# Kernel tuning notes

Measured on AMD Instinct MI355X. Metric: run time of the kernel, lower is better.

## Reference

```python
import jax, jax.numpy as jnp
import numpy as np

N, E, D = 50000, 1600000, 128


def _mk_w(key, shape):
    return jax.random.normal(key, shape, dtype=jnp.float32) * 0.05


def setup_inputs() -> dict:
    key = jax.random.key(0)
    ks = jax.random.split(key, 32)
    inp = {
        'x_in': jax.random.normal(ks[0], (N, D), dtype=jnp.float32),
        'rows': jax.random.randint(ks[1], (E,), 0, N, dtype=jnp.int64 if jax.config.jax_enable_x64 else jnp.int32),
        'cols': jax.random.randint(ks[2], (E,), 0, N, dtype=jnp.int64 if jax.config.jax_enable_x64 else jnp.int32),
        'vals': jax.random.uniform(ks[3], (E,), dtype=jnp.float32),
    }
    names = ['m1_W1', 'm1_W2', 'm2_W1', 'm2_W2', 'Wu1', 'Wu2', 'Wr1', 'Wr2', 'Wo1', 'Wo2']
    for i, n in enumerate(names):
        inp[n] = _mk_w(ks[4 + i], (D, D))
        inp[n.replace('W', 'b')] = jnp.zeros((D,), dtype=jnp.float32)
    return inp


def _mlp2(x, W1, b1, W2, b2):
    # 2-layer MLP: Linear -> ReLU -> Linear
    return jax.nn.relu(x @ W1 + b1) @ W2 + b2


def reference(x_in, rows, cols, vals,
              m1_W1, m1_b1, m1_W2, m1_b2,
              m2_W1, m2_b1, m2_W2, m2_b2,
              Wu1, bu1, Wu2, bu2,
              Wr1, br1, Wr2, br2,
              Wo1, bo1, Wo2, bo2):
    x = _mlp2(x_in, m1_W1, m1_b1, m1_W2, m1_b2)            # [N, D]
    # sparse COO spmm: out[i] = sum_e vals[e] * x[cols[e]] for rows[e] == i
    msgs = vals[:, None] * x[cols]                          # [E, D]
    agg = jax.ops.segment_sum(msgs, rows, num_segments=N)   # [N, D]
    out = _mlp2(agg, m2_W1, m2_b1, m2_W2, m2_b2)
    z = jax.nn.sigmoid(out @ Wu1 + bu1 + x @ Wu2 + bu2)
    r = jax.nn.sigmoid(out @ Wr1 + br1 + x @ Wr2 + br2)
    h = jnp.tanh(out @ Wo1 + bo1 + (r * x) @ Wo2 + bo2)
    return (1.0 - z) * x + z * h
```

## Files before the change

kernel.cpp:

```cpp
#include <hip/hip_runtime.h>

#define DD 128
#define BSHIFT 7
#define BROWS 128
#define MS_TILE 4096
#define MS_EPT 8
#define STAGE_CAP 6144

typedef __attribute__((ext_vector_type(8))) short short8;
typedef __attribute__((ext_vector_type(4))) float f32x4;
typedef unsigned short u16;
typedef unsigned int u32;

__device__ __forceinline__ u16 f2bf(float f) {
  u32 u = __builtin_bit_cast(u32, f);
  u += 0x7fffu + ((u >> 16) & 1u);
  return (u16)(u >> 16);
}
__device__ __forceinline__ float bf2f(u16 s) {
  u32 u = ((u32)s) << 16;
  return __builtin_bit_cast(float, u);
}
__device__ __forceinline__ float f16val(u32 cv) {
  return (float)__builtin_bit_cast(_Float16, (u16)(cv & 0xffffu));
}
__device__ __forceinline__ float sigmoidf_(float v) { return 1.f / (1.f + __expf(-v)); }
__device__ __forceinline__ float tanhf_(float v) {
  float e = __expf(-2.f * v);
  return (1.f - e) / (1.f + e);
}

struct WPtrs { const float* w[10]; };

__global__ void pack_weights(WPtrs wp, u16* __restrict__ bp) {
  const float* W = wp.w[blockIdx.x];
  u16* out = bp + (size_t)blockIdx.x * 16384;
  for (int o = threadIdx.x; o < 16384; o += blockDim.x) {
    int e = o & 7, lane = (o >> 3) & 63, nt = (o >> 9) & 7, ks = o >> 12;
    int k = ks * 32 + (lane >> 4) * 8 + e;
    int c = (lane & 15) + nt * 16;
    out[o] = f2bf(W[k * DD + c]);
  }
}

__global__ __launch_bounds__(512) void multisplit(const int* __restrict__ rows,
                                                  const int* __restrict__ cols,
                                                  const float* __restrict__ vals,
                                                  int* __restrict__ cursor,
                                                  uint2* __restrict__ recs,
                                                  int E, int NB, int cap) {
  __shared__ u32 hist[512];
  __shared__ u32 scan_tmp[512];
  __shared__ u32 hbase[512];
  __shared__ int gbase[512];
  __shared__ u32 rankc[512];
  __shared__ uint2 stage[MS_TILE];
  const int t = threadIdx.x;
  const int tile0 = blockIdx.x * MS_TILE;
  hist[t] = 0;
  rankc[t] = 0;
  __syncthreads();
  int myb[MS_EPT];
  u32 mycv[MS_EPT], myrow[MS_EPT];
#pragma unroll
  for (int j = 0; j < MS_EPT; ++j) {
    int e = tile0 + j * 512 + t;
    if (e < E) {
      int r = rows[e];
      int b = r >> BSHIFT;
      myb[j] = b;
      myrow[j] = (u32)r;
      _Float16 hf = (_Float16)vals[e];
      mycv[j] = ((u32)cols[e] << 16) | (u32)__builtin_bit_cast(u16, hf);
      atomicAdd(&hist[b], 1u);
    } else {
      myb[j] = -1;
    }
  }
  __syncthreads();
  u32 v = hist[t];
  scan_tmp[t] = v;
  __syncthreads();
  for (int o = 1; o < 512; o <<= 1) {
    u32 x = (t >= o) ? scan_tmp[t - o] : 0;
    __syncthreads();
    scan_tmp[t] += x;
    __syncthreads();
  }
  hbase[t] = scan_tmp[t] - v;
  if (t < NB && v > 0) gbase[t] = atomicAdd(&cursor[t], (int)v);
  __syncthreads();
#pragma unroll
  for (int j = 0; j < MS_EPT; ++j) {
    if (myb[j] >= 0) {
      u32 rk = atomicAdd(&rankc[myb[j]], 1u);
      stage[hbase[myb[j]] + rk].x = mycv[j];
      stage[hbase[myb[j]] + rk].y = myrow[j];
    }
  }
  __syncthreads();
  int cnt = E - tile0;
  cnt = cnt < MS_TILE ? cnt : MS_TILE;
  for (int k = t; k < cnt; k += 512) {
    uint2 rec = stage[k];
    int b = (int)(rec.y >> BSHIFT);
    int off = gbase[b] + (k - (int)hbase[b]);
    if (off < cap) recs[(size_t)b * cap + off] = rec;
  }
}

__global__ __launch_bounds__(512) void bucket_csr(const uint2* __restrict__ recs,
                                                  const int* __restrict__ cursor,
                                                  u32* __restrict__ recs2,
                                                  int* __restrict__ rowstart,
                                                  int* __restrict__ rowcnt, int n, int cap) {
  __shared__ int hist[BROWS];
  __shared__ int sc[BROWS];
  __shared__ int hbase[BROWS];
  __shared__ u32 rank[BROWS];
  __shared__ u32 stage[STAGE_CAP];
  const int t = threadIdx.x;
  const int b = blockIdx.x;
  int cnt = cursor[b];
  cnt = cnt < cap ? cnt : cap;
  const uint2* rb = recs + (size_t)b * cap;
  if (t < BROWS) { hist[t] = 0; rank[t] = 0; }
  __syncthreads();
  for (int i = t; i < cnt; i += 512) atomicAdd(&hist[rb[i].y & (BROWS - 1)], 1);
  __syncthreads();
  if (t < BROWS) sc[t] = hist[t];
  __syncthreads();
  for (int o = 1; o < BROWS; o <<= 1) {
    int x = (t >= o && t < BROWS) ? sc[t - o] : 0;
    __syncthreads();
    if (t < BROWS) sc[t] += x;
    __syncthreads();
  }
  if (t < BROWS) {
    hbase[t] = sc[t] - hist[t];
    int r = (b << BSHIFT) + t;
    if (r < n) {
      rowstart[r] = b * cap + hbase[t];
      rowcnt[r] = hist[t];
    }
  }
  __syncthreads();
  for (int i = t; i < cnt; i += 512) {
    uint2 rec = rb[i];
    int lr = (int)(rec.y & (BROWS - 1));
    u32 p = atomicAdd(&rank[lr], 1u);
    stage[hbase[lr] + p] = rec.x;
  }
  __syncthreads();
  u32* ob = recs2 + (size_t)b * cap;
  for (int i = t; i < cnt; i += 512) ob[i] = stage[i];
}

__global__ void spmm_agg(const int* __restrict__ rowstart, const int* __restrict__ rowcnt,
                         const u32* __restrict__ recs2, const u16* __restrict__ xb,
                         u16* __restrict__ aggb, int n) {
  int row = blockIdx.x * 4 + (threadIdx.x >> 6);
  int lane = threadIdx.x & 63;
  if (row >= n) return;
  int s = rowstart[row];
  int e2 = s + rowcnt[row];
  float a0 = 0.f, a1 = 0.f;
  int j = s;
  for (; j + 3 < e2; j += 4) {
    u32 pk0 = recs2[j], pk1 = recs2[j + 1], pk2 = recs2[j + 2], pk3 = recs2[j + 3];
    u32 x0 = *reinterpret_cast<const u32*>(xb + (size_t)(pk0 >> 16) * DD + lane * 2);
    u32 x1 = *reinterpret_cast<const u32*>(xb + (size_t)(pk1 >> 16) * DD + lane * 2);
    u32 x2 = *reinterpret_cast<const u32*>(xb + (size_t)(pk2 >> 16) * DD + lane * 2);
    u32 x3 = *reinterpret_cast<const u32*>(xb + (size_t)(pk3 >> 16) * DD + lane * 2);
    float v0 = f16val(pk0), v1 = f16val(pk1), v2 = f16val(pk2), v3 = f16val(pk3);
    a0 += v0 * bf2f((u16)(x0 & 0xffff)) + v1 * bf2f((u16)(x1 & 0xffff)) +
          v2 * bf2f((u16)(x2 & 0xffff)) + v3 * bf2f((u16)(x3 & 0xffff));
    a1 += v0 * bf2f((u16)(x0 >> 16)) + v1 * bf2f((u16)(x1 >> 16)) +
          v2 * bf2f((u16)(x2 >> 16)) + v3 * bf2f((u16)(x3 >> 16));
  }
  for (; j < e2; ++j) {
    u32 pk = recs2[j];
    u32 x0 = *reinterpret_cast<const u32*>(xb + (size_t)(pk >> 16) * DD + lane * 2);
    float v0 = f16val(pk);
    a0 += v0 * bf2f((u16)(x0 & 0xffff));
    a1 += v0 * bf2f((u16)(x0 >> 16));
  }
  u32 o = ((u32)f2bf(a1) << 16) | (u32)f2bf(a0);
  *reinterpret_cast<u32*>(aggb + (size_t)row * DD + lane * 2) = o;
}

template <int ASRC>
__global__ __launch_bounds__(256) void mlp_fused(const void* __restrict__ Ain,
                                                 const u16* __restrict__ W1p,
                                                 const float* __restrict__ b1,
                                                 const u16* __restrict__ W2p,
                                                 const float* __restrict__ b2,
                                                 u16* __restrict__ outB, int n) {
  __shared__ u16 sm[32][136];
  const int lane = threadIdx.x & 63;
  const int wid = threadIdx.x >> 6;
  const int m = wid >> 1, c = wid & 1;
  const int row0 = blockIdx.x * 32 + m * 16;
  const int ar = lane & 15, ak = (lane >> 4) * 8;
  const int crow = 4 * (lane >> 4), ccol = lane & 15;

  f32x4 acc[4];
#pragma unroll
  for (int t = 0; t < 4; ++t) acc[t] = f32x4{0.f, 0.f, 0.f, 0.f};

#pragma unroll
  for (int ks = 0; ks < 4; ++ks) {
    short8 a;
    int r = row0 + ar;
    r = r < n ? r : n - 1;
    if (ASRC == 0) {
      const float* Ap = (const float*)Ain + (size_t)r * DD + ks * 32 + ak;
      float4 f0 = *reinterpret_cast<const float4*>(Ap);
      float4 f1 = *reinterpret_cast<const float4*>(Ap + 4);
      short8 tv;
      tv[0] = (short)f2bf(f0.x); tv[1] = (short)f2bf(f0.y);
      tv[2] = (short)f2bf(f0.z); tv[3] = (short)f2bf(f0.w);
      tv[4] = (short)f2bf(f1.x); tv[5] = (short)f2bf(f1.y);
      tv[6] = (short)f2bf(f1.z); tv[7] = (short)f2bf(f1.w);
      a = tv;
    } else {
      a = *reinterpret_cast<const short8*>((const u16*)Ain + (size_t)r * DD + ks * 32 + ak);
    }
#pragma unroll
    for (int nt4 = 0; nt4 < 4; ++nt4) {
      int nt = c * 4 + nt4;
      short8 bfr = *reinterpret_cast<const short8*>(W1p + (((ks * 8 + nt) * 64 + lane) * 8));
      acc[nt4] = __builtin_amdgcn_mfma_f32_16x16x32_bf16(a, bfr, acc[nt4], 0, 0, 0);
    }
  }
#pragma unroll
  for (int nt4 = 0; nt4 < 4; ++nt4) {
    int col = (c * 4 + nt4) * 16 + ccol;
    float bsv = b1[col];
#pragma unroll
    for (int e = 0; e < 4; ++e) {
      float v = acc[nt4][e] + bsv;
      v = v > 0.f ? v : 0.f;
      sm[m * 16 + crow + e][col] = f2bf(v);
    }
  }
  __syncthreads();

  f32x4 acc2[4];
#pragma unroll
  for (int t = 0; t < 4; ++t) acc2[t] = f32x4{0.f, 0.f, 0.f, 0.f};
#pragma unroll
  for (int ks = 0; ks < 4; ++ks) {
    short8 a2 = *reinterpret_cast<const short8*>(&sm[m * 16 + ar][ks * 32 + ak]);
#pragma unroll
    for (int nt4 = 0; nt4 < 4; ++nt4) {
      int nt = c * 4 + nt4;
      short8 bfr = *reinterpret_cast<const short8*>(W2p + (((ks * 8 + nt) * 64 + lane) * 8));
      acc2[nt4] = __builtin_amdgcn_mfma_f32_16x16x32_bf16(a2, bfr, acc2[nt4], 0, 0, 0);
    }
  }
#pragma unroll
  for (int nt4 = 0; nt4 < 4; ++nt4) {
    int col = (c * 4 + nt4) * 16 + ccol;
    float bsv = b2[col];
#pragma unroll
    for (int e = 0; e < 4; ++e) {
      int r = row0 + crow + e;
      if (r < n) outB[(size_t)r * DD + col] = f2bf(acc2[nt4][e] + bsv);
    }
  }
}

__global__ __launch_bounds__(256) void gates_final(
    const u16* __restrict__ Ao, const u16* __restrict__ Ax, const u16* __restrict__ Wu1p,
    const u16* __restrict__ Wu2p, const u16* __restrict__ Wr1p, const u16* __restrict__ Wr2p,
    const u16* __restrict__ Wo1p, const u16* __restrict__ Wo2p, const float* __restrict__ bu1,
    const float* __restrict__ bu2, const float* __restrict__ br1, const float* __restrict__ br2,
    const float* __restrict__ bo1, const float* __restrict__ bo2, float* __restrict__ out,
    int n) {
  __shared__ u16 sm[32][136];
  const int lane = threadIdx.x & 63;
  const int wid = threadIdx.x >> 6;
  const int m = wid >> 1, c = wid & 1;
  const int row0 = blockIdx.x * 32 + m * 16;
  const int ar = lane & 15, ak = (lane >> 4) * 8;
  const int crow = 4 * (lane >> 4), ccol = lane & 15;

  f32x4 aZ[4], aR[4], aO[4];
#pragma unroll
  for (int t = 0; t < 4; ++t) {
    aZ[t] = f32x4{0.f, 0.f, 0.f, 0.f};
    aR[t] = f32x4{0.f, 0.f, 0.f, 0.f};
    aO[t] = f32x4{0.f, 0.f, 0.f, 0.f};
  }
#pragma unroll
  for (int ks = 0; ks < 4; ++ks) {
    int r = row0 + ar;
    r = r < n ? r : n - 1;
    short8 ao = *reinterpret_cast<const short8*>(Ao + (size_t)r * DD + ks * 32 + ak);
    short8 ax = *reinterpret_cast<const short8*>(Ax + (size_t)r * DD + ks * 32 + ak);
#pragma unroll
    for (int nt4 = 0; nt4 < 4; ++nt4) {
      int nt = c * 4 + nt4;
      size_t bo = (size_t)(((ks * 8 + nt) * 64 + lane) * 8);
      short8 b1 = *reinterpret_cast<const short8*>(Wu1p + bo);
      short8 b2 = *reinterpret_cast<const short8*>(Wu2p + bo);
      short8 b3 = *reinterpret_cast<const short8*>(Wr1p + bo);
      short8 b4 = *reinterpret_cast<const short8*>(Wr2p + bo);
      short8 b5 = *reinterpret_cast<const short8*>(Wo1p + bo);
      aZ[nt4] = __builtin_amdgcn_mfma_f32_16x16x32_bf16(ao, b1, aZ[nt4], 0, 0, 0);
      aZ[nt4] = __builtin_amdgcn_mfma_f32_16x16x32_bf16(ax, b2, aZ[nt4], 0, 0, 0);
      aR[nt4] = __builtin_amdgcn_mfma_f32_16x16x32_bf16(ao, b3, aR[nt4], 0, 0, 0);
      aR[nt4] = __builtin_amdgcn_mfma_f32_16x16x32_bf16(ax, b4, aR[nt4], 0, 0, 0);
      aO[nt4] = __builtin_amdgcn_mfma_f32_16x16x32_bf16(ao, b5, aO[nt4], 0, 0, 0);
    }
  }
#pragma unroll
  for (int nt4 = 0; nt4 < 4; ++nt4) {
    int col = (c * 4 + nt4) * 16 + ccol;
    float bz = bu1[col] + bu2[col];
    float br_ = br1[col] + br2[col];
    float bo_ = bo1[col];
#pragma unroll
    for (int e = 0; e < 4; ++e) {
      int r = row0 + crow + e;
      float z = sigmoidf_(aZ[nt4][e] + bz);
      float rr = sigmoidf_(aR[nt4][e] + br_);
      aZ[nt4][e] = z;
      aO[nt4][e] = aO[nt4][e] + bo_;
      float xv = 0.f;
      if (r < n) xv = bf2f(Ax[(size_t)r * DD + col]);
      sm[m * 16 + crow + e][col] = f2bf(rr * xv);
    }
  }
  __syncthreads();

  f32x4 acc2[4];
#pragma unroll
  for (int t = 0; t < 4; ++t) acc2[t] = f32x4{0.f, 0.f, 0.f, 0.f};
#pragma unroll
  for (int ks = 0; ks < 4; ++ks) {
    short8 a2 = *reinterpret_cast<const short8*>(&sm[m * 16 + ar][ks * 32 + ak]);
#pragma unroll
    for (int nt4 = 0; nt4 < 4; ++nt4) {
      int nt = c * 4 + nt4;
      short8 bfr = *reinterpret_cast<const short8*>(Wo2p + (((ks * 8 + nt) * 64 + lane) * 8));
      acc2[nt4] = __builtin_amdgcn_mfma_f32_16x16x32_bf16(a2, bfr, acc2[nt4], 0, 0, 0);
    }
  }
#pragma unroll
  for (int nt4 = 0; nt4 < 4; ++nt4) {
    int col = (c * 4 + nt4) * 16 + ccol;
    float bo2v = bo2[col];
#pragma unroll
    for (int e = 0; e < 4; ++e) {
      int r = row0 + crow + e;
      if (r < n) {
        size_t idx = (size_t)r * DD + col;
        float oi = acc2[nt4][e] + bo2v + aO[nt4][e];
        float h = tanhf_(oi);
        float z = aZ[nt4][e];
        float xv = bf2f(Ax[idx]);
        out[idx] = (1.f - z) * xv + z * h;
      }
    }
  }
}

extern "C" void kernel_launch(void* const* d_in, const int* in_sizes, int n_in,
                              void* d_out, int out_size, void* d_ws, size_t ws_size,
                              hipStream_t stream) {
  const int n = in_sizes[0] / DD;
  const int E = in_sizes[1];
  const float* x_in = (const float*)d_in[0];
  const int* rows = (const int*)d_in[1];
  const int* cols = (const int*)d_in[2];
  const float* vals = (const float*)d_in[3];
  const float* Wm[10];
  const float* Bm[10];
  for (int i = 0; i < 10; ++i) {
    Wm[i] = (const float*)d_in[4 + 2 * i];
    Bm[i] = (const float*)d_in[5 + 2 * i];
  }

  const int NB = (n + BROWS - 1) >> BSHIFT;
  int cap = (((E / NB) * 5) / 4 + 511) & ~511;
  cap = cap < STAGE_CAP ? cap : STAGE_CAP;

  char* base = (char*)d_ws;
  size_t off = 0;
  auto alloc = [&](size_t bytes) -> char* {
    char* p = base + off;
    off += (bytes + 255) & ~(size_t)255;
    return p;
  };
  u16* wpack = (u16*)alloc((size_t)10 * 16384 * 2);
  u16* x_b = (u16*)alloc((size_t)n * DD * 2);
  u16* agg_b = (u16*)alloc((size_t)n * DD * 2);
  int* cursor = (int*)alloc((size_t)NB * 4);
  int* rowstart = (int*)alloc((size_t)n * 4);
  int* rowcnt = (int*)alloc((size_t)n * 4);
  uint2* recs = (uint2*)alloc((size_t)NB * cap * 8);
  u32* recs2 = (u32*)alloc((size_t)NB * cap * 4);
  (void)ws_size;
  (void)n_in;
  (void)out_size;

  hipMemsetAsync(cursor, 0, (size_t)NB * 4, stream);
  WPtrs wp;
  for (int i = 0; i < 10; ++i) wp.w[i] = Wm[i];
  pack_weights<<<10, 256, 0, stream>>>(wp, wpack);
  multisplit<<<(E + MS_TILE - 1) / MS_TILE, 512, 0, stream>>>(rows, cols, vals, cursor, recs, E,
                                                             NB, cap);
  bucket_csr<<<NB, 512, 0, stream>>>(recs, cursor, recs2, rowstart, rowcnt, n, cap);
  int gblocks = (n + 31) / 32;
  mlp_fused<0><<<gblocks, 256, 0, stream>>>(x_in, wpack + 0 * 16384, Bm[0], wpack + 1 * 16384,
                                            Bm[1], x_b, n);
  spmm_agg<<<(n + 3) / 4, 256, 0, stream>>>(rowstart, rowcnt, recs2, x_b, agg_b, n);
  mlp_fused<1><<<gblocks, 256, 0, stream>>>(agg_b, wpack + 2 * 16384, Bm[2], wpack + 3 * 16384,
                                            Bm[3], agg_b, n);
  gates_final<<<gblocks, 256, 0, stream>>>(
      agg_b, x_b, wpack + 4 * 16384, wpack + 5 * 16384, wpack + 6 * 16384, wpack + 7 * 16384,
      wpack + 8 * 16384, wpack + 9 * 16384, Bm[4], Bm[5], Bm[6], Bm[7], Bm[8], Bm[9],
      (float*)d_out, n);
}
```

Before: 306.1 us.

## Fuse second MLP into gates kernel and split SpMM wave across edge pairs

The second MLP (m2) is merged into the gates kernel. Its output now stays in shared memory instead of making a round trip through global memory, and one kernel launch goes away. The SpMM aggregation now handles two edges at a time per wave: each half-wave loads 8 bytes per lane for one edge, the loop is unrolled by 16, and the halves are combined with a cross-lane shuffle. This raises the number of gathers in flight per wave at the cost of extra shuffles and some redundant record loads.

```diff
diff --git a/kernel.cpp b/kernel.cpp
--- a/kernel.cpp
+++ b/kernel.cpp
@@ -162,31 +162,49 @@
   int row = blockIdx.x * 4 + (threadIdx.x >> 6);
   int lane = threadIdx.x & 63;
   if (row >= n) return;
-  int s = rowstart[row];
-  int e2 = s + rowcnt[row];
-  float a0 = 0.f, a1 = 0.f;
-  int j = s;
-  for (; j + 3 < e2; j += 4) {
-    u32 pk0 = recs2[j], pk1 = recs2[j + 1], pk2 = recs2[j + 2], pk3 = recs2[j + 3];
-    u32 x0 = *reinterpret_cast<const u32*>(xb + (size_t)(pk0 >> 16) * DD + lane * 2);
-    u32 x1 = *reinterpret_cast<const u32*>(xb + (size_t)(pk1 >> 16) * DD + lane * 2);
-    u32 x2 = *reinterpret_cast<const u32*>(xb + (size_t)(pk2 >> 16) * DD + lane * 2);
-    u32 x3 = *reinterpret_cast<const u32*>(xb + (size_t)(pk3 >> 16) * DD + lane * 2);
-    float v0 = f16val(pk0), v1 = f16val(pk1), v2 = f16val(pk2), v3 = f16val(pk3);
-    a0 += v0 * bf2f((u16)(x0 & 0xffff)) + v1 * bf2f((u16)(x1 & 0xffff)) +
-          v2 * bf2f((u16)(x2 & 0xffff)) + v3 * bf2f((u16)(x3 & 0xffff));
-    a1 += v0 * bf2f((u16)(x0 >> 16)) + v1 * bf2f((u16)(x1 >> 16)) +
-          v2 * bf2f((u16)(x2 >> 16)) + v3 * bf2f((u16)(x3 >> 16));
-  }
-  for (; j < e2; ++j) {
-    u32 pk = recs2[j];
-    u32 x0 = *reinterpret_cast<const u32*>(xb + (size_t)(pk >> 16) * DD + lane * 2);
-    float v0 = f16val(pk);
-    a0 += v0 * bf2f((u16)(x0 & 0xffff));
-    a1 += v0 * bf2f((u16)(x0 >> 16));
-  }
-  u32 o = ((u32)f2bf(a1) << 16) | (u32)f2bf(a0);
-  *reinterpret_cast<u32*>(aggb + (size_t)row * DD + lane * 2) = o;
+  const int s = rowstart[row];
+  const int cnt = rowcnt[row];
+  const int hi = lane >> 5;
+  const int l32 = lane & 31;
+  float a0 = 0.f, a1 = 0.f, a2 = 0.f, a3 = 0.f;
+  int j = 0;
+#define SPMM_PAIR(P)                                                                   \
+  {                                                                                    \
+    u32 pk0 = recs2[s + j + 2 * (P)];                                                  \
+    u32 pk1 = recs2[s + j + 2 * (P) + 1];                                              \
+    u32 pk = hi ? pk1 : pk0;                                                           \
+    uint2 xv = *(reinterpret_cast<const uint2*>(xb + (size_t)(pk >> 16) * DD) + l32);  \
+    float vv = f16val(pk);                                                             \
+    a0 += vv * bf2f((u16)(xv.x & 0xffffu));                                            \
+    a1 += vv * bf2f((u16)(xv.x >> 16));                                                \
+    a2 += vv * bf2f((u16)(xv.y & 0xffffu));                                            \
+    a3 += vv * bf2f((u16)(xv.y >> 16));                                                \
+  }
+  for (; j + 15 < cnt; j += 16) {
+    SPMM_PAIR(0) SPMM_PAIR(1) SPMM_PAIR(2) SPMM_PAIR(3)
+    SPMM_PAIR(4) SPMM_PAIR(5) SPMM_PAIR(6) SPMM_PAIR(7)
+  }
+  for (; j + 1 < cnt; j += 2) { SPMM_PAIR(0) }
+  if (j < cnt) {
+    u32 pk0 = recs2[s + j];
+    uint2 xv = *(reinterpret_cast<const uint2*>(xb + (size_t)(pk0 >> 16) * DD) + l32);
+    float vv = hi ? 0.f : f16val(pk0);
+    a0 += vv * bf2f((u16)(xv.x & 0xffffu));
+    a1 += vv * bf2f((u16)(xv.x >> 16));
+    a2 += vv * bf2f((u16)(xv.y & 0xffffu));
+    a3 += vv * bf2f((u16)(xv.y >> 16));
+  }
+#undef SPMM_PAIR
+  a0 += __shfl_xor(a0, 32, 64);
+  a1 += __shfl_xor(a1, 32, 64);
+  a2 += __shfl_xor(a2, 32, 64);
+  a3 += __shfl_xor(a3, 32, 64);
+  if (!hi) {
+    uint2 o;
+    o.x = ((u32)f2bf(a1) << 16) | (u32)f2bf(a0);
+    o.y = ((u32)f2bf(a3) << 16) | (u32)f2bf(a2);
+    *reinterpret_cast<uint2*>(aggb + (size_t)row * DD + l32 * 4) = o;
+  }
 }
 
 template <int ASRC>
@@ -271,13 +289,14 @@
   }
 }
 
-__global__ __launch_bounds__(256) void gates_final(
-    const u16* __restrict__ Ao, const u16* __restrict__ Ax, const u16* __restrict__ Wu1p,
-    const u16* __restrict__ Wu2p, const u16* __restrict__ Wr1p, const u16* __restrict__ Wr2p,
-    const u16* __restrict__ Wo1p, const u16* __restrict__ Wo2p, const float* __restrict__ bu1,
-    const float* __restrict__ bu2, const float* __restrict__ br1, const float* __restrict__ br2,
-    const float* __restrict__ bo1, const float* __restrict__ bo2, float* __restrict__ out,
-    int n) {
+__global__ __launch_bounds__(256) void mlp2_gates_final(
+    const u16* __restrict__ Agg, const u16* __restrict__ Ax, const u16* __restrict__ W3p,
+    const float* __restrict__ b3, const u16* __restrict__ W4p, const float* __restrict__ b4,
+    const u16* __restrict__ Wu1p, const u16* __restrict__ Wu2p, const u16* __restrict__ Wr1p,
+    const u16* __restrict__ Wr2p, const u16* __restrict__ Wo1p, const u16* __restrict__ Wo2p,
+    const float* __restrict__ bu1, const float* __restrict__ bu2, const float* __restrict__ br1,
+    const float* __restrict__ br2, const float* __restrict__ bo1, const float* __restrict__ bo2,
+    float* __restrict__ out, int n) {
   __shared__ u16 sm[32][136];
   const int lane = threadIdx.x & 63;
   const int wid = threadIdx.x >> 6;
@@ -286,6 +305,57 @@
   const int ar = lane & 15, ak = (lane >> 4) * 8;
   const int crow = 4 * (lane >> 4), ccol = lane & 15;
 
+  f32x4 acc[4];
+#pragma unroll
+  for (int t = 0; t < 4; ++t) acc[t] = f32x4{0.f, 0.f, 0.f, 0.f};
+#pragma unroll
+  for (int ks = 0; ks < 4; ++ks) {
+    int r = row0 + ar;
+    r = r < n ? r : n - 1;
+    short8 a = *reinterpret_cast<const short8*>(Agg + (size_t)r * DD + ks * 32 + ak);
+#pragma unroll
+    for (int nt4 = 0; nt4 < 4; ++nt4) {
+      int nt = c * 4 + nt4;
+      short8 bfr = *reinterpret_cast<const short8*>(W3p + (((ks * 8 + nt) * 64 + lane) * 8));
+      acc[nt4] = __builtin_amdgcn_mfma_f32_16x16x32_bf16(a, bfr, acc[nt4], 0, 0, 0);
+    }
+  }
+#pragma unroll
+  for (int nt4 = 0; nt4 < 4; ++nt4) {
+    int col = (c * 4 + nt4) * 16 + ccol;
+    float bsv = b3[col];
+#pragma unroll
+    for (int e = 0; e < 4; ++e) {
+      float v = acc[nt4][e] + bsv;
+      v = v > 0.f ? v : 0.f;
+      sm[m * 16 + crow + e][col] = f2bf(v);
+    }
+  }
+  __syncthreads();
+
+#pragma unroll
+  for (int t = 0; t < 4; ++t) acc[t] = f32x4{0.f, 0.f, 0.f, 0.f};
+#pragma unroll
+  for (int ks = 0; ks < 4; ++ks) {
+    short8 a2 = *reinterpret_cast<const short8*>(&sm[m * 16 + ar][ks * 32 + ak]);
+#pragma unroll
+    for (int nt4 = 0; nt4 < 4; ++nt4) {
+      int nt = c * 4 + nt4;
+      short8 bfr = *reinterpret_cast<const short8*>(W4p + (((ks * 8 + nt) * 64 + lane) * 8));
+      acc[nt4] = __builtin_amdgcn_mfma_f32_16x16x32_bf16(a2, bfr, acc[nt4], 0, 0, 0);
+    }
+  }
+  __syncthreads();
+#pragma unroll
+  for (int nt4 = 0; nt4 < 4; ++nt4) {
+    int col = (c * 4 + nt4) * 16 + ccol;
+    float bsv = b4[col];
+#pragma unroll
+    for (int e = 0; e < 4; ++e)
+      sm[m * 16 + crow + e][col] = f2bf(acc[nt4][e] + bsv);
+  }
+  __syncthreads();
+
   f32x4 aZ[4], aR[4], aO[4];
 #pragma unroll
   for (int t = 0; t < 4; ++t) {
@@ -297,7 +367,7 @@
   for (int ks = 0; ks < 4; ++ks) {
     int r = row0 + ar;
     r = r < n ? r : n - 1;
-    short8 ao = *reinterpret_cast<const short8*>(Ao + (size_t)r * DD + ks * 32 + ak);
+    short8 ao = *reinterpret_cast<const short8*>(&sm[m * 16 + ar][ks * 32 + ak]);
     short8 ax = *reinterpret_cast<const short8*>(Ax + (size_t)r * DD + ks * 32 + ak);
 #pragma unroll
     for (int nt4 = 0; nt4 < 4; ++nt4) {
@@ -305,16 +375,17 @@
       size_t bo = (size_t)(((ks * 8 + nt) * 64 + lane) * 8);
       short8 b1 = *reinterpret_cast<const short8*>(Wu1p + bo);
       short8 b2 = *reinterpret_cast<const short8*>(Wu2p + bo);
-      short8 b3 = *reinterpret_cast<const short8*>(Wr1p + bo);
-      short8 b4 = *reinterpret_cast<const short8*>(Wr2p + bo);
+      short8 b3f = *reinterpret_cast<const short8*>(Wr1p + bo);
+      short8 b4f = *reinterpret_cast<const short8*>(Wr2p + bo);
       short8 b5 = *reinterpret_cast<const short8*>(Wo1p + bo);
       aZ[nt4] = __builtin_amdgcn_mfma_f32_16x16x32_bf16(ao, b1, aZ[nt4], 0, 0, 0);
       aZ[nt4] = __builtin_amdgcn_mfma_f32_16x16x32_bf16(ax, b2, aZ[nt4], 0, 0, 0);
-      aR[nt4] = __builtin_amdgcn_mfma_f32_16x16x32_bf16(ao, b3, aR[nt4], 0, 0, 0);
-      aR[nt4] = __builtin_amdgcn_mfma_f32_16x16x32_bf16(ax, b4, aR[nt4], 0, 0, 0);
+      aR[nt4] = __builtin_amdgcn_mfma_f32_16x16x32_bf16(ao, b3f, aR[nt4], 0, 0, 0);
+      aR[nt4] = __builtin_amdgcn_mfma_f32_16x16x32_bf16(ax, b4f, aR[nt4], 0, 0, 0);
       aO[nt4] = __builtin_amdgcn_mfma_f32_16x16x32_bf16(ao, b5, aO[nt4], 0, 0, 0);
     }
   }
+  __syncthreads();
 #pragma unroll
   for (int nt4 = 0; nt4 < 4; ++nt4) {
     int col = (c * 4 + nt4) * 16 + ccol;
@@ -417,10 +488,8 @@
   mlp_fused<0><<<gblocks, 256, 0, stream>>>(x_in, wpack + 0 * 16384, Bm[0], wpack + 1 * 16384,
                                             Bm[1], x_b, n);
   spmm_agg<<<(n + 3) / 4, 256, 0, stream>>>(rowstart, rowcnt, recs2, x_b, agg_b, n);
-  mlp_fused<1><<<gblocks, 256, 0, stream>>>(agg_b, wpack + 2 * 16384, Bm[2], wpack + 3 * 16384,
-                                            Bm[3], agg_b, n);
-  gates_final<<<gblocks, 256, 0, stream>>>(
-      agg_b, x_b, wpack + 4 * 16384, wpack + 5 * 16384, wpack + 6 * 16384, wpack + 7 * 16384,
-      wpack + 8 * 16384, wpack + 9 * 16384, Bm[4], Bm[5], Bm[6], Bm[7], Bm[8], Bm[9],
-      (float*)d_out, n);
-}
+  mlp2_gates_final<<<gblocks, 256, 0, stream>>>(
+      agg_b, x_b, wpack + 2 * 16384, Bm[2], wpack + 3 * 16384, Bm[3], wpack + 4 * 16384,
+      wpack + 5 * 16384, wpack + 6 * 16384, wpack + 7 * 16384, wpack + 8 * 16384,
+      wpack + 9 * 16384, Bm[4], Bm[5], Bm[6], Bm[7], Bm[8], Bm[9], (float*)d_out, n);
+}
```

Measured after the change: 287.8 us. 6.0% less time.
